# Kernel optimization log

Measured on AMD Instinct MI355X. Metric: run time of the kernel, lower is better.

## Reference

```python
import jax, jax.numpy as jnp
import numpy as np

T, E, IN, OUT, A, R = 16384, 8, 1024, 1024, 8, 16  # tokens, experts, d_in, d_out, adapters, lora rank


def prepare_routing(x, indices, num_groups):
    """Sort tokens by group index; return sorted x, per-group counts, unsort map, sorted ids."""
    sort_idx = jnp.argsort(indices)  # stable sort keeps within-group order
    x_sorted = x[sort_idx]
    group_sizes = jnp.bincount(indices, length=num_groups).astype(jnp.int32)
    unsort_indices = jnp.argsort(sort_idx)
    return x_sorted, group_sizes, unsort_indices, indices[sort_idx]


def setup_inputs() -> dict:
    key = jax.random.key(0)
    ks = jax.random.split(key, 6)
    # tokens pre-sorted by expert: group_sizes must sum to T exactly
    expert_ids = jnp.sort(jax.random.randint(ks[0], (T,), 0, E))
    group_sizes = jnp.bincount(expert_ids, length=E).astype(jnp.int32)
    x = jax.random.normal(ks[1], (T, IN), jnp.float32)
    adapter_indices_sorted = jax.random.randint(ks[2], (T,), 0, A)
    weight = jax.random.normal(ks[3], (E, IN, OUT), jnp.float32) * 0.02
    lora_A = jax.random.normal(ks[4], (A, E, IN, R), jnp.float32) * 0.02
    lora_B = jax.random.normal(ks[5], (A, E, R, OUT), jnp.float32) * 0.02
    lora_scaling = jnp.ones((A,), jnp.float32)
    return {
        "x": x,
        "group_sizes": group_sizes,
        "adapter_indices_sorted": adapter_indices_sorted,
        "weight": weight,
        "lora_A": lora_A,
        "lora_B": lora_B,
        "lora_scaling": lora_scaling,
    }


def reference(x, group_sizes, adapter_indices_sorted, weight, lora_A, lora_B, lora_scaling):
    # base grouped GEMM over experts: [T,IN] x [E,IN,OUT] -> [T,OUT]
    base_out = jax.lax.ragged_dot(x, weight, group_sizes)

    # per-token expert id from contiguous group sizes
    expert_ids = jnp.repeat(jnp.arange(E), group_sizes, total_repeat_length=T)
    flattened = expert_ids * A + adapter_indices_sorted  # expert-major (E,A) group id

    # flatten adapters x experts into E*A groups (expert-major to match flattened ids)
    A_mat = lora_A.transpose(1, 0, 2, 3).reshape(E * A, IN, R)
    B_mat = lora_B.transpose(1, 0, 2, 3).reshape(E * A, R, OUT)

    x_sorted, combined_gs, unsort_indices, _ = prepare_routing(x, flattened, E * A)
    inter = jax.lax.ragged_dot(x_sorted, A_mat, combined_gs)          # [T,R]
    lora_out_sorted = jax.lax.ragged_dot(inter, B_mat, combined_gs)   # [T,OUT]
    lora_out = lora_out_sorted[unsort_indices]
    lora_out = lora_out * lora_scaling[adapter_indices_sorted][:, None]
    return base_out + lora_out
```

## Files before the change

kernel.cpp:

```cpp
#include <hip/hip_runtime.h>

#define T_TOK 16384
#define NEXP 8
#define DIN 1024
#define DOUT 1024
#define NADP 8
#define RANK 16
#define NGRP 64
#define MAXTILES 135
#define MAXP1 520
#define BK 64

typedef float f32x4 __attribute__((ext_vector_type(4)));
typedef float f32x16 __attribute__((ext_vector_type(16)));
typedef __bf16 bf16x8 __attribute__((ext_vector_type(8)));

typedef __attribute__((address_space(3))) void lds_void;
typedef __attribute__((address_space(1))) void g_void;

static __device__ __forceinline__ unsigned short f2bf(float f) {
    union { float f; unsigned u; } c; c.f = f;
    unsigned r = c.u + 0x7FFFu + ((c.u >> 16) & 1u);
    return (unsigned short)(r >> 16);
}

#define XB2 2048
#define NBW 2048
__global__ __launch_bounds__(256) void k_convert_all(const float* __restrict__ x,
                                                     const float* __restrict__ W,
                                                     const float* __restrict__ lA,
                                                     const float* __restrict__ lB,
                                                     unsigned short* __restrict__ xb,
                                                     unsigned short* __restrict__ Wt,
                                                     unsigned short* __restrict__ Agt,
                                                     unsigned short* __restrict__ Blt) {
    __shared__ __attribute__((aligned(16))) unsigned short lds_u[16 * 1032];
    int b = blockIdx.x;
    int t = threadIdx.x;
    if (b < XB2) {
        const size_t total = (size_t)(T_TOK + 128) * DIN / 4;
        const size_t conv  = (size_t)T_TOK * DIN / 4;
        size_t gid = (size_t)b * 256 + t;
#pragma unroll
        for (int it = 0; it < 9; it++) {
            size_t u = gid + (size_t)it * (XB2 * 256);
            if (u < total) {
                ushort4 o;
                if (u < conv) {
                    float4 v = *(const float4*)(x + u * 4);
                    o.x = f2bf(v.x); o.y = f2bf(v.y); o.z = f2bf(v.z); o.w = f2bf(v.w);
                } else {
                    o.x = 0; o.y = 0; o.z = 0; o.w = 0;
                }
                *(ushort4*)(xb + u * 4) = o;
            }
        }
    } else if (b < XB2 + NBW) {
        int idx = b - XB2;
        int e = idx >> 8;
        int k0 = ((idx >> 4) & 15) * 64, n0 = (idx & 15) * 64;
        const float* We = W + (size_t)e * DIN * DOUT;
        unsigned short* Wte = Wt + (size_t)e * DIN * DOUT;
        unsigned* lds32 = (unsigned*)lds_u;
        int kp = t >> 3;
        int nc = (t & 7) * 8;
        const float* r0 = We + (size_t)(k0 + 2 * kp) * DOUT + n0 + nc;
        const float* r1 = r0 + DOUT;
        float4 a0 = *(const float4*)r0, a1 = *(const float4*)(r0 + 4);
        float4 c0 = *(const float4*)r1, c1 = *(const float4*)(r1 + 4);
        lds32[(nc + 0) * 34 + kp] = (unsigned)f2bf(a0.x) | ((unsigned)f2bf(c0.x) << 16);
        lds32[(nc + 1) * 34 + kp] = (unsigned)f2bf(a0.y) | ((unsigned)f2bf(c0.y) << 16);
        lds32[(nc + 2) * 34 + kp] = (unsigned)f2bf(a0.z) | ((unsigned)f2bf(c0.z) << 16);
        lds32[(nc + 3) * 34 + kp] = (unsigned)f2bf(a0.w) | ((unsigned)f2bf(c0.w) << 16);
        lds32[(nc + 4) * 34 + kp] = (unsigned)f2bf(a1.x) | ((unsigned)f2bf(c1.x) << 16);
        lds32[(nc + 5) * 34 + kp] = (unsigned)f2bf(a1.y) | ((unsigned)f2bf(c1.y) << 16);
        lds32[(nc + 6) * 34 + kp] = (unsigned)f2bf(a1.z) | ((unsigned)f2bf(c1.z) << 16);
        lds32[(nc + 7) * 34 + kp] = (unsigned)f2bf(a1.w) | ((unsigned)f2bf(c1.w) << 16);
        __syncthreads();
        int n = t >> 2, kq = (t & 3) * 8;
        uint2 d0 = *(const uint2*)&lds32[n * 34 + kq + 0];
        uint2 d1 = *(const uint2*)&lds32[n * 34 + kq + 2];
        uint2 d2 = *(const uint2*)&lds32[n * 34 + kq + 4];
        uint2 d3 = *(const uint2*)&lds32[n * 34 + kq + 6];
        uint4 v0; v0.x = d0.x; v0.y = d0.y; v0.z = d1.x; v0.w = d1.y;
        uint4 v1; v1.x = d2.x; v1.y = d2.y; v1.z = d3.x; v1.w = d3.y;
        *(uint4*)(Wte + (size_t)(n0 + n) * DIN + k0 + kq * 2) = v0;
        *(uint4*)(Wte + (size_t)(n0 + n) * DIN + k0 + kq * 2 + 8) = v1;
    } else if (b < XB2 + NBW + NGRP) {
        int g = b - (XB2 + NBW);
        int a = g & 7, e = g >> 3;
        const float* src = lA + (size_t)(a * NEXP + e) * DIN * RANK;
#pragma unroll
        for (int it = 0; it < 4; it++) {
            int k = it * 256 + t;
            const float4* p = (const float4*)(src + (size_t)k * RANK);
            float4 v0 = p[0], v1 = p[1], v2 = p[2], v3 = p[3];
            lds_u[0 * 1032 + k] = f2bf(v0.x);  lds_u[1 * 1032 + k] = f2bf(v0.y);
            lds_u[2 * 1032 + k] = f2bf(v0.z);  lds_u[3 * 1032 + k] = f2bf(v0.w);
            lds_u[4 * 1032 + k] = f2bf(v1.x);  lds_u[5 * 1032 + k] = f2bf(v1.y);
            lds_u[6 * 1032 + k] = f2bf(v1.z);  lds_u[7 * 1032 + k] = f2bf(v1.w);
            lds_u[8 * 1032 + k] = f2bf(v2.x);  lds_u[9 * 1032 + k] = f2bf(v2.y);
            lds_u[10 * 1032 + k] = f2bf(v2.z); lds_u[11 * 1032 + k] = f2bf(v2.w);
            lds_u[12 * 1032 + k] = f2bf(v3.x); lds_u[13 * 1032 + k] = f2bf(v3.y);
            lds_u[14 * 1032 + k] = f2bf(v3.z); lds_u[15 * 1032 + k] = f2bf(v3.w);
        }
        __syncthreads();
        unsigned short* dst = Agt + (size_t)g * RANK * DIN;
        int r = t >> 4, ks = (t & 15) * 64;
#pragma unroll
        for (int j = 0; j < 8; j++)
            *(uint4*)(dst + r * DIN + ks + j * 8) = *(const uint4*)&lds_u[r * 1032 + ks + j * 8];
    } else {
        int idx = b - (XB2 + NBW + NGRP);
        int e = idx >> 3, nc = idx & 7;
        int k = t >> 1, half = t & 1;
        int a = k >> 4, r = k & 15;
        const float* src = lB + ((size_t)(a * NEXP + e) * RANK + r) * DOUT + nc * 128 + half * 64;
#pragma unroll
        for (int j = 0; j < 16; j++) {
            float4 v = *(const float4*)(src + j * 4);
            int nl = half * 64 + j * 4;
            lds_u[k * 129 + nl + 0] = f2bf(v.x);
            lds_u[k * 129 + nl + 1] = f2bf(v.y);
            lds_u[k * 129 + nl + 2] = f2bf(v.z);
            lds_u[k * 129 + nl + 3] = f2bf(v.w);
        }
        __syncthreads();
        int nl = t >> 1, kh = t & 1;
        unsigned short* dst = Blt + ((size_t)(e * 1024 + nc * 128 + nl)) * 128 + kh * 64;
#pragma unroll
        for (int g2 = 0; g2 < 8; g2++) {
            uint4 pv;
            unsigned short s0 = lds_u[(kh * 64 + g2 * 8 + 0) * 129 + nl];
            unsigned short s1 = lds_u[(kh * 64 + g2 * 8 + 1) * 129 + nl];
            unsigned short s2 = lds_u[(kh * 64 + g2 * 8 + 2) * 129 + nl];
            unsigned short s3 = lds_u[(kh * 64 + g2 * 8 + 3) * 129 + nl];
            unsigned short s4 = lds_u[(kh * 64 + g2 * 8 + 4) * 129 + nl];
            unsigned short s5 = lds_u[(kh * 64 + g2 * 8 + 5) * 129 + nl];
            unsigned short s6 = lds_u[(kh * 64 + g2 * 8 + 6) * 129 + nl];
            unsigned short s7 = lds_u[(kh * 64 + g2 * 8 + 7) * 129 + nl];
            pv.x = (unsigned)s0 | ((unsigned)s1 << 16);
            pv.y = (unsigned)s2 | ((unsigned)s3 << 16);
            pv.z = (unsigned)s4 | ((unsigned)s5 << 16);
            pv.w = (unsigned)s6 | ((unsigned)s7 << 16);
            *(uint4*)(dst + g2 * 8) = pv;
        }
    }
}

__global__ __launch_bounds__(256) void k_pass1(const unsigned short* __restrict__ xb,
                                               const unsigned short* __restrict__ Agt,
                                               const int* __restrict__ gs,
                                               const int* __restrict__ aidx,
                                               const float* __restrict__ scal,
                                               unsigned short* __restrict__ interb) {
    int bid = blockIdx.x;
    int e = -1, m0 = 0, valid = 0;
    {
        int acc_t = 0, base = 0;
#pragma unroll
        for (int ee = 0; ee < NEXP; ee++) {
            int sz = gs[ee];
            int nt = (sz + 31) >> 5;
            if (e < 0 && bid < acc_t + nt) {
                int loc = bid - acc_t;
                e = ee; m0 = base + (loc << 5);
                int v = sz - (loc << 5); valid = v > 32 ? 32 : v;
            }
            acc_t += nt; base += sz;
        }
    }
    if (e < 0) return;

    int t = threadIdx.x;
    int lane = t & 63, w = t >> 6;
    int ln = lane & 15, q = lane >> 4;

    const unsigned short* A0 = Agt + ((size_t)(e * NADP + 2 * w) * RANK + ln) * DIN + q * 8;
    const unsigned short* A1 = A0 + (size_t)RANK * DIN;
    const unsigned short* X0 = xb + (size_t)(m0 + ln) * DIN + q * 8;

    f32x4 acc[2][2];
#pragma unroll
    for (int i = 0; i < 2; i++) {
        acc[i][0] = (f32x4){0.f, 0.f, 0.f, 0.f};
        acc[i][1] = (f32x4){0.f, 0.f, 0.f, 0.f};
    }

#pragma unroll 4
    for (int k0 = 0; k0 < DIN; k0 += 32) {
        bf16x8 b0 = *(const bf16x8*)(A0 + k0);
        bf16x8 b1 = *(const bf16x8*)(A1 + k0);
#pragma unroll
        for (int rg = 0; rg < 2; rg++) {
            bf16x8 af = *(const bf16x8*)(X0 + (size_t)(rg * 16) * DIN + k0);
            acc[rg][0] = __builtin_amdgcn_mfma_f32_16x16x32_bf16(b0, af, acc[rg][0], 0, 0, 0);
            acc[rg][1] = __builtin_amdgcn_mfma_f32_16x16x32_bf16(b1, af, acc[rg][1], 0, 0, 0);
        }
    }

    float s0 = scal[2 * w], s1 = scal[2 * w + 1];
#pragma unroll
    for (int rg = 0; rg < 2; rg++) {
        int tr = rg * 16 + ln;
        if (tr < valid) {
            int tok = m0 + tr;
            int a = aidx[tok];
            if (a == 2 * w) {
                f32x4 v = acc[rg][0];
                ushort4 u;
                u.x = f2bf(s0 * v[0]); u.y = f2bf(s0 * v[1]);
                u.z = f2bf(s0 * v[2]); u.w = f2bf(s0 * v[3]);
                *(ushort4*)(interb + (size_t)tok * RANK + q * 4) = u;
            } else if (a == 2 * w + 1) {
                f32x4 v = acc[rg][1];
                ushort4 u;
                u.x = f2bf(s1 * v[0]); u.y = f2bf(s1 * v[1]);
                u.z = f2bf(s1 * v[2]); u.w = f2bf(s1 * v[3]);
                *(ushort4*)(interb + (size_t)tok * RANK + q * 4) = u;
            }
        }
    }
}

__global__ __launch_bounds__(256) void k_gemm(const unsigned short* __restrict__ xb,
                                              const unsigned short* __restrict__ wt,
                                              const int* __restrict__ gs,
                                              const unsigned short* __restrict__ interb,
                                              const int* __restrict__ aidx,
                                              const unsigned short* __restrict__ Blt,
                                              float* __restrict__ out) {
    __shared__ __attribute__((aligned(16))) unsigned short smem[32768];
    int tileid = blockIdx.y;
    int e = -1, m0 = 0, valid = 0;
    {
        int acc_t = 0, base = 0;
#pragma unroll
        for (int ee = 0; ee < NEXP; ee++) {
            int sz = gs[ee];
            int nt = (sz + 127) >> 7;
            if (e < 0 && tileid < acc_t + nt) {
                int loc = tileid - acc_t;
                e = ee; m0 = base + (loc << 7);
                int v = sz - (loc << 7); valid = v > 128 ? 128 : v;
            }
            acc_t += nt; base += sz;
        }
    }
    if (e < 0) return;
    int n0 = blockIdx.x * 128;

    int t = threadIdx.x;
    int lane = t & 63;
    int wave = t >> 6;
    int wm = wave >> 1, wn = wave & 1;
    int r32 = lane & 31, hi = lane >> 5;

    const unsigned short* wte = wt + (size_t)e * DIN * DOUT;

    f32x16 acc[2][2];
#pragma unroll
    for (int i = 0; i < 2; i++)
#pragma unroll
        for (int j = 0; j < 2; j++) acc[i][j] = (f32x16)(0.f);

    int srow[4], skoff[4];
#pragma unroll
    for (int j = 0; j < 4; j++) {
        srow[j]  = j * 32 + wave * 8 + (lane >> 3);
        skoff[j] = ((lane & 7) ^ (srow[j] & 7)) * 8;
    }

    auto STAGE = [&](int buf, int k0) {
#pragma unroll
        for (int j = 0; j < 4; j++) {
            __builtin_amdgcn_global_load_lds(
                (const g_void*)(xb + (size_t)(m0 + srow[j]) * DIN + k0 + skoff[j]),
                (lds_void*)((char*)smem + buf * 32768 + j * 4096 + wave * 1024), 16, 0, 0);
            __builtin_amdgcn_global_load_lds(
                (const g_void*)(wte + (size_t)(n0 + srow[j]) * DIN + k0 + skoff[j]),
                (lds_void*)((char*)smem + buf * 32768 + 16384 + j * 4096 + wave * 1024), 16, 0, 0);
        }
    };

    auto COMPUTE = [&](int buf) {
        const char* Ab = (const char*)smem + buf * 32768;
        const char* Bb = Ab + 16384;
#pragma unroll
        for (int kf = 0; kf < 4; kf++) {
            int kc = kf * 2 + hi;
            int slot = kc ^ (r32 & 7);
            bf16x8 af[2], bfr[2];
#pragma unroll
            for (int mi = 0; mi < 2; mi++) {
                int row = wm * 64 + mi * 32 + r32;
                af[mi] = *(const bf16x8*)(Ab + row * 128 + slot * 16);
            }
#pragma unroll
            for (int ni = 0; ni < 2; ni++) {
                int row = wn * 64 + ni * 32 + r32;
                bfr[ni] = *(const bf16x8*)(Bb + row * 128 + slot * 16);
            }
#pragma unroll
            for (int mi = 0; mi < 2; mi++)
#pragma unroll
                for (int ni = 0; ni < 2; ni++)
                    acc[mi][ni] = __builtin_amdgcn_mfma_f32_32x32x16_bf16(af[mi], bfr[ni], acc[mi][ni], 0, 0, 0);
        }
    };

    STAGE(0, 0);
    __syncthreads();
    int cur = 0;
    for (int k0 = BK; k0 < DIN; k0 += BK) {
        STAGE(cur ^ 1, k0);
        COMPUTE(cur);
        __syncthreads();
        cur ^= 1;
    }
    COMPUTE(cur);

    __syncthreads();
    {
        int row = t >> 1, h = t & 1;
        int rs = row & 15;
        uint4 z = {0u, 0u, 0u, 0u};
        uint4 payload = z;
        int pslot = -1;
        if (row < valid) {
            int tok = m0 + row;
            int a = aidx[tok];
            payload = *(const uint4*)(interb + (size_t)tok * RANK + h * 8);
            pslot = a * 2 + h;
        }
#pragma unroll
        for (int l2 = 0; l2 < 8; l2++) {
            int l = l2 * 2 + h;
            int phys = l ^ rs;
            *(uint4*)((char*)smem + row * 256 + phys * 16) = (l == pslot) ? payload : z;
        }
    }
    __syncthreads();
#pragma unroll
    for (int kf = 0; kf < 8; kf++) {
        int kc = kf * 2 + hi;
        bf16x8 af[2], bfr[2];
#pragma unroll
        for (int ni = 0; ni < 2; ni++) {
            int n = wn * 64 + ni * 32 + r32;
            bfr[ni] = *(const bf16x8*)(Blt + ((size_t)(e * 1024 + n0 + n)) * 128 + kc * 8);
        }
#pragma unroll
        for (int mi = 0; mi < 2; mi++) {
            int row = wm * 64 + mi * 32 + r32;
            int slot = kc ^ (r32 & 15);
            af[mi] = *(const bf16x8*)((const char*)smem + row * 256 + slot * 16);
        }
#pragma unroll
        for (int mi = 0; mi < 2; mi++)
#pragma unroll
            for (int ni = 0; ni < 2; ni++)
                acc[mi][ni] = __builtin_amdgcn_mfma_f32_32x32x16_bf16(af[mi], bfr[ni], acc[mi][ni], 0, 0, 0);
    }

#pragma unroll
    for (int mi = 0; mi < 2; mi++) {
#pragma unroll
        for (int r = 0; r < 16; r++) {
            int row32 = (r & 3) + 8 * (r >> 2) + 4 * hi;
            int row_l = wm * 64 + mi * 32 + row32;
            if (row_l < valid) {
                float* orow = out + (size_t)(m0 + row_l) * DOUT + n0 + wn * 64 + r32;
#pragma unroll
                for (int ni = 0; ni < 2; ni++)
                    orow[ni * 32] = acc[mi][ni][r];
            }
        }
    }
}

extern "C" void kernel_launch(void* const* d_in, const int* in_sizes, int n_in,
                              void* d_out, int out_size, void* d_ws, size_t ws_size,
                              hipStream_t stream) {
    (void)in_sizes; (void)n_in; (void)out_size; (void)ws_size;
    const float* x    = (const float*)d_in[0];
    const int*   gs   = (const int*)d_in[1];
    const int*   aidx = (const int*)d_in[2];
    const float* W    = (const float*)d_in[3];
    const float* lA   = (const float*)d_in[4];
    const float* lB   = (const float*)d_in[5];
    const float* scal = (const float*)d_in[6];
    float* out = (float*)d_out;

    char* ws = (char*)d_ws;
    unsigned short* xb     = (unsigned short*)ws;        size_t o = 33816576;
    unsigned short* wt     = (unsigned short*)(ws + o);  o += 16777216;
    unsigned short* Agt    = (unsigned short*)(ws + o);  o += 2097152;
    unsigned short* Blt    = (unsigned short*)(ws + o);  o += 2097152;
    unsigned short* interb = (unsigned short*)(ws + o);  o += 524288;

    k_convert_all<<<XB2 + NBW + NGRP + 64, 256, 0, stream>>>(x, W, lA, lB, xb, wt, Agt, Blt);
    k_pass1<<<MAXP1, 256, 0, stream>>>(xb, Agt, gs, aidx, scal, interb);
    k_gemm<<<dim3(8, MAXTILES), 256, 0, stream>>>(xb, wt, gs, interb, aidx, Blt, out);
}
```

Before: 276.3 us.

## Keep two K-stages in flight with vmcnt waits, remap tiles per XCD, raise MFMA priority

The main K loop of the grouped GEMM now issues the first two stages up front. Each step uses `s_waitcnt vmcnt` plus a raw `s_barrier` instead of `__syncthreads`, so one global-to-LDS stage stays in flight while the current buffer is computed. The block index is remapped so each XCD gets a contiguous run of M tiles across all N columns, which should improve L2 reuse of the x rows. The compute section is also wrapped in `s_setprio` to favour the MFMA waves. The risk is that the hand-written wait counts and barrier placement are fragile, and the epilogue's safety from an LDS race depends on the last step using buffer 1.

Result: faster. 264.9 us (-4.1%).

```diff
diff --git a/kernel.cpp b/kernel.cpp
--- a/kernel.cpp
+++ b/kernel.cpp
@@ -7,9 +7,9 @@
 #define NADP 8
 #define RANK 16
 #define NGRP 64
-#define MAXTILES 135
 #define MAXP1 520
 #define BK 64
+#define NKSTEP 16
 
 typedef float f32x4 __attribute__((ext_vector_type(4)));
 typedef float f32x16 __attribute__((ext_vector_type(16)));
@@ -231,7 +231,13 @@
                                               const unsigned short* __restrict__ Blt,
                                               float* __restrict__ out) {
     __shared__ __attribute__((aligned(16))) unsigned short smem[32768];
-    int tileid = blockIdx.y;
+
+    int id = blockIdx.y * 8 + blockIdx.x;
+    int xcd = id & 7;
+    int j = id >> 3;
+    int tileid = xcd * 17 + (j >> 3);
+    int n0 = (j & 7) * 128;
+
     int e = -1, m0 = 0, valid = 0;
     {
         int acc_t = 0, base = 0;
@@ -248,7 +254,6 @@
         }
     }
     if (e < 0) return;
-    int n0 = blockIdx.x * 128;
 
     int t = threadIdx.x;
     int lane = t & 63;
@@ -262,30 +267,31 @@
 #pragma unroll
     for (int i = 0; i < 2; i++)
 #pragma unroll
-        for (int j = 0; j < 2; j++) acc[i][j] = (f32x16)(0.f);
+        for (int j2 = 0; j2 < 2; j2++) acc[i][j2] = (f32x16)(0.f);
 
     int srow[4], skoff[4];
 #pragma unroll
-    for (int j = 0; j < 4; j++) {
-        srow[j]  = j * 32 + wave * 8 + (lane >> 3);
-        skoff[j] = ((lane & 7) ^ (srow[j] & 7)) * 8;
+    for (int j3 = 0; j3 < 4; j3++) {
+        srow[j3]  = j3 * 32 + wave * 8 + (lane >> 3);
+        skoff[j3] = ((lane & 7) ^ (srow[j3] & 7)) * 8;
     }
 
     auto STAGE = [&](int buf, int k0) {
 #pragma unroll
-        for (int j = 0; j < 4; j++) {
+        for (int j3 = 0; j3 < 4; j3++) {
             __builtin_amdgcn_global_load_lds(
-                (const g_void*)(xb + (size_t)(m0 + srow[j]) * DIN + k0 + skoff[j]),
-                (lds_void*)((char*)smem + buf * 32768 + j * 4096 + wave * 1024), 16, 0, 0);
+                (const g_void*)(xb + (size_t)(m0 + srow[j3]) * DIN + k0 + skoff[j3]),
+                (lds_void*)((char*)smem + buf * 32768 + j3 * 4096 + wave * 1024), 16, 0, 0);
             __builtin_amdgcn_global_load_lds(
-                (const g_void*)(wte + (size_t)(n0 + srow[j]) * DIN + k0 + skoff[j]),
-                (lds_void*)((char*)smem + buf * 32768 + 16384 + j * 4096 + wave * 1024), 16, 0, 0);
+                (const g_void*)(wte + (size_t)(n0 + srow[j3]) * DIN + k0 + skoff[j3]),
+                (lds_void*)((char*)smem + buf * 32768 + 16384 + j3 * 4096 + wave * 1024), 16, 0, 0);
         }
     };
 
     auto COMPUTE = [&](int buf) {
         const char* Ab = (const char*)smem + buf * 32768;
         const char* Bb = Ab + 16384;
+        __builtin_amdgcn_s_setprio(1);
 #pragma unroll
         for (int kf = 0; kf < 4; kf++) {
             int kc = kf * 2 + hi;
@@ -307,20 +313,23 @@
                 for (int ni = 0; ni < 2; ni++)
                     acc[mi][ni] = __builtin_amdgcn_mfma_f32_32x32x16_bf16(af[mi], bfr[ni], acc[mi][ni], 0, 0, 0);
         }
+        __builtin_amdgcn_s_setprio(0);
     };
 
     STAGE(0, 0);
-    __syncthreads();
-    int cur = 0;
-    for (int k0 = BK; k0 < DIN; k0 += BK) {
-        STAGE(cur ^ 1, k0);
-        COMPUTE(cur);
-        __syncthreads();
-        cur ^= 1;
-    }
-    COMPUTE(cur);
-
-    __syncthreads();
+    STAGE(1, BK);
+#pragma unroll
+    for (int ts = 0; ts < NKSTEP; ts++) {
+        if (ts < NKSTEP - 1) asm volatile("s_waitcnt vmcnt(8)" ::: "memory");
+        else                 asm volatile("s_waitcnt vmcnt(0)" ::: "memory");
+        __builtin_amdgcn_s_barrier();
+        COMPUTE(ts & 1);
+        if (ts < NKSTEP - 2) {
+            __builtin_amdgcn_s_barrier();
+            STAGE(ts & 1, (ts + 2) * BK);
+        }
+    }
+
     {
         int row = t >> 1, h = t & 1;
         int rs = row & 15;
@@ -401,5 +410,5 @@
 
     k_convert_all<<<XB2 + NBW + NGRP + 64, 256, 0, stream>>>(x, W, lA, lB, xb, wt, Agt, Blt);
     k_pass1<<<MAXP1, 256, 0, stream>>>(xb, Agt, gs, aidx, scal, interb);
-    k_gemm<<<dim3(8, MAXTILES), 256, 0, stream>>>(xb, wt, gs, interb, aidx, Blt, out);
+    k_gemm<<<dim3(8, 136), 256, 0, stream>>>(xb, wt, gs, interb, aidx, Blt, out);
 }
```
